# Kernel optimization log

Hardware: AMD Instinct MI355X
Metric: run time of the kernel (lower is better)

The kernel has to match this reference:

```python
import jax, jax.numpy as jnp
import numpy as np

N_NODES = 50000
NEG_SLOPE = 0.2  # PyG GATConv default leaky_relu slope


def setup_inputs() -> dict:
    key = jax.random.key(0)
    ks = jax.random.split(key, 12)
    N, E, D_IN, H = N_NODES, 1200000, 128, 64
    sd_in = 1.0 / np.sqrt(D_IN)
    sd_h = 1.0 / np.sqrt(H)
    return {
        "x": jax.random.normal(ks[0], (N, D_IN), jnp.float32),
        "src": jax.random.randint(ks[1], (E,), 0, N, jnp.int32),
        "dst": jax.random.randint(ks[2], (E,), 0, N, jnp.int32),
        "W1_src": jax.random.normal(ks[3], (D_IN, H), jnp.float32) * sd_in,
        "W1_dst": jax.random.normal(ks[4], (D_IN, H), jnp.float32) * sd_in,
        "a1_src": jax.random.normal(ks[5], (H,), jnp.float32) * sd_h,
        "a1_dst": jax.random.normal(ks[6], (H,), jnp.float32) * sd_h,
        "b1": jnp.zeros((H,), jnp.float32),
        "W2_src": jax.random.normal(ks[7], (H, H), jnp.float32) * sd_h,
        "W2_dst": jax.random.normal(ks[8], (H, H), jnp.float32) * sd_h,
        "a2_src": jax.random.normal(ks[9], (H,), jnp.float32) * sd_h,
        "a2_dst": jax.random.normal(ks[10], (H,), jnp.float32) * sd_h,
        "b2": jnp.zeros((H,), jnp.float32),
    }


def _gat_layer(x, src, dst, W_src, W_dst, att_src, att_dst, bias):
    N = x.shape[0]
    h_src = x @ W_src            # [N, H] transformed source features
    h_dst = x @ W_dst            # [N, H] transformed destination features
    alpha_src = h_src @ att_src  # [N]
    alpha_dst = h_dst @ att_dst  # [N]
    # edge-wise attention logits (gather), edge j -> i: e = lrelu(a_src[j] + a_dst[i])
    e = jax.nn.leaky_relu(alpha_src[src] + alpha_dst[dst], NEG_SLOPE)  # [E]
    # segment softmax over incoming edges of each destination node
    m = jax.ops.segment_max(e, dst, num_segments=N)          # [N]
    ex = jnp.exp(e - m[dst])                                  # [E]
    denom = jax.ops.segment_sum(ex, dst, num_segments=N)     # [N]
    alpha = ex / denom[dst]                                   # [E]
    # weighted scatter-add aggregation
    msgs = h_src[src] * alpha[:, None]                        # [E, H]
    out = jax.ops.segment_sum(msgs, dst, num_segments=N)     # [N, H]
    return out + bias


def reference(x, src, dst, W1_src, W1_dst, a1_src, a1_dst, b1,
              W2_src, W2_dst, a2_src, a2_dst, b2):
    h = jnp.tanh(_gat_layer(x, src, dst, W1_src, W1_dst, a1_src, a1_dst, b1))
    h = jnp.tanh(_gat_layer(h, src, dst, W2_src, W2_dst, a2_src, a2_dst, b2))
    return h
```

## Files before the change

### kernel.cpp

```cpp
#include <hip/hip_runtime.h>
#include <hip/hip_bf16.h>

#define NEG_SLOPE 0.2f
#define EPB 4096
#define NHB 64

typedef __attribute__((ext_vector_type(8))) short short8v;
typedef __attribute__((ext_vector_type(4))) float f32x4;

__device__ inline float blo(unsigned u) { return __uint_as_float(u << 16); }
__device__ inline float bhi(unsigned u) { return __uint_as_float(u & 0xffff0000u); }
__device__ inline unsigned short bf16bits(float f) {
    __hip_bfloat16 b = __float2bfloat16(f);
    return *(unsigned short*)&b;
}
__device__ inline unsigned pack2bf(float e, float o) {
    return ((unsigned)bf16bits(o) << 16) | (unsigned)bf16bits(e);
}

template <int K>
__device__ inline void stage_sBt(unsigned short* sBt,
                                 const float* __restrict__ W_src,
                                 const float* __restrict__ a_src,
                                 const float* __restrict__ W_dst,
                                 const float* __restrict__ a_dst, int tid) {
    constexpr int PAD = K + 8;
    for (int i = tid; i < 64 * K; i += 256) {
        int k = i >> 6, j = i & 63;
        sBt[j * PAD + k] = bf16bits(W_src[i]);
    }
    for (int i = tid; i < 2 * K; i += 256) {
        int which = (i >= K) ? 1 : 0;
        int k = i - which * K;
        const float* Wr = (which ? W_dst : W_src) + k * 64;
        const float* av = which ? a_dst : a_src;
        float s = 0.f;
        #pragma unroll
        for (int j = 0; j < 64; ++j) s += Wr[j] * av[j];
        sBt[(64 + which) * PAD + k] = bf16bits(s);
    }
    for (int i = tid; i < 14 * K; i += 256) {
        int j = 66 + i / K, k = i % K;
        sBt[j * PAD + k] = 0;
    }
}

template <int K>
__device__ inline void nt_mfma_body(const unsigned short* sBt,
                                    const unsigned short* sX,
                                    int rowblockbase,
                                    unsigned* __restrict__ hb_out,
                                    float* __restrict__ alpha_src,
                                    float* __restrict__ alpha_dst,
                                    int N, int tid) {
    constexpr int PAD = K + 8;
    int wid = tid >> 6, l = tid & 63;
    int jcol = l & 15;

    f32x4 acc[5];
    #pragma unroll
    for (int t = 0; t < 5; ++t) acc[t] = (f32x4){0.f, 0.f, 0.f, 0.f};

    const unsigned short* xrow = &sX[(wid * 16 + (l & 15)) * PAD + (l >> 4) * 8];
    #pragma unroll
    for (int kt = 0; kt < K / 32; ++kt) {
        short8v a = *(const short8v*)(xrow + kt * 32);
        int kbase = kt * 32 + (l >> 4) * 8;
        #pragma unroll
        for (int t = 0; t < 5; ++t) {
            short8v b = *(const short8v*)&sBt[(t * 16 + jcol) * PAD + kbase];
            acc[t] = __builtin_amdgcn_mfma_f32_16x16x32_bf16(a, b, acc[t], 0, 0, 0);
        }
    }

    int rbase = rowblockbase + wid * 16 + (l >> 4) * 4;
    #pragma unroll
    for (int t = 0; t < 4; ++t) {
        #pragma unroll
        for (int r = 0; r < 4; ++r) {
            float v = acc[t][r];
            float w = __shfl_xor(v, 1);
            int row = rbase + r;
            if (!(l & 1) && row < N)
                hb_out[(size_t)row * 32 + t * 8 + (jcol >> 1)] = pack2bf(v, w);
        }
    }
    #pragma unroll
    for (int r = 0; r < 4; ++r) {
        int row = rbase + r;
        if (row < N) {
            if (jcol == 0) alpha_src[row] = acc[4][r];
            if (jcol == 1) alpha_dst[row] = acc[4][r];
        }
    }
}

__global__ __launch_bounds__(256) void fused_nt1_hist(
    const float* __restrict__ x,
    const float* __restrict__ W_src, const float* __restrict__ a_src,
    const float* __restrict__ W_dst, const float* __restrict__ a_dst,
    unsigned* __restrict__ hb_out, float* __restrict__ alpha_src,
    float* __restrict__ alpha_dst, int N,
    const int* __restrict__ dst, int* __restrict__ partials, int E, int ntb) {
    constexpr int K = 128, PAD = K + 8;
    __shared__ unsigned short sBt[80 * PAD];
    __shared__ unsigned short sX[64 * PAD];
    __shared__ int lh[256];
    int tid = threadIdx.x;

    if ((int)blockIdx.x >= ntb) {
        int bh = blockIdx.x - ntb;
        lh[tid] = 0;
        __syncthreads();
        for (int e = bh * 256 + tid; e < E; e += NHB * 256)
            atomicAdd(&lh[dst[e] >> 8], 1);
        __syncthreads();
        partials[bh * 256 + tid] = lh[tid];
        return;
    }

    stage_sBt<K>(sBt, W_src, a_src, W_dst, a_dst, tid);
    for (int idx = tid; idx < 64 * K / 4; idx += 256) {
        int row = (idx * 4) / K, col = (idx * 4) % K;
        int g = blockIdx.x * 64 + row;
        const float4 f = *(const float4*)(x + (size_t)((g < N) ? g : N - 1) * K + col);
        unsigned short* d = &sX[row * PAD + col];
        d[0] = bf16bits(f.x); d[1] = bf16bits(f.y);
        d[2] = bf16bits(f.z); d[3] = bf16bits(f.w);
    }
    __syncthreads();
    nt_mfma_body<K>(sBt, sX, blockIdx.x * 64, hb_out, alpha_src, alpha_dst, N, tid);
}

__global__ __launch_bounds__(256) void bucket_scan(const int* __restrict__ partials,
                                                   int* __restrict__ bucket_base,
                                                   int* __restrict__ bucket_cursor) {
    __shared__ int tmp[256];
    int tid = threadIdx.x;
    int v = 0;
    #pragma unroll 8
    for (int b = 0; b < NHB; ++b) v += partials[b * 256 + tid];
    tmp[tid] = v;
    __syncthreads();
    for (int off = 1; off < 256; off <<= 1) {
        int t = (tid >= off) ? tmp[tid - off] : 0;
        __syncthreads();
        tmp[tid] += t;
        __syncthreads();
    }
    int excl = tmp[tid] - v;
    bucket_base[tid] = excl;
    bucket_cursor[tid] = excl;
    if (tid == 255) bucket_base[256] = tmp[255];
}

__global__ __launch_bounds__(256) void bucket_scatter(const int* __restrict__ src,
                                                      const int* __restrict__ dst,
                                                      int* __restrict__ bucket_cursor,
                                                      unsigned* __restrict__ ebuf, int E) {
    __shared__ int lhist[256];
    __shared__ int lbase[256];
    int tid = threadIdx.x;
    lhist[tid] = 0;
    __syncthreads();
    int base = blockIdx.x * EPB;
    int bkt[16], rank[16];
    unsigned pack[16];
    #pragma unroll
    for (int i = 0; i < 16; ++i) {
        int e = base + i * 256 + tid;
        bkt[i] = -1;
        if (e < E) {
            int d = dst[e], s = src[e];
            bkt[i]  = d >> 8;
            pack[i] = ((unsigned)(d & 255) << 16) | (unsigned)s;
            rank[i] = atomicAdd(&lhist[bkt[i]], 1);
        }
    }
    __syncthreads();
    int cnt = lhist[tid];
    if (cnt) lbase[tid] = atomicAdd(&bucket_cursor[tid], cnt);
    __syncthreads();
    #pragma unroll
    for (int i = 0; i < 16; ++i)
        if (bkt[i] >= 0) ebuf[lbase[bkt[i]] + rank[i]] = pack[i];
}

__global__ __launch_bounds__(256) void bucket_build(const unsigned* __restrict__ ebuf,
                                                    const int* __restrict__ bucket_base,
                                                    int* __restrict__ row_ptr,
                                                    int* __restrict__ csr_src,
                                                    int N, int E) {
    __shared__ int deg[256];
    __shared__ int cur[256];
    __shared__ int tmp[256];
    int b = blockIdx.x, tid = threadIdx.x;
    int ebase = bucket_base[b], eend = bucket_base[b + 1];
    deg[tid] = 0;
    __syncthreads();
    for (int e = ebase + tid; e < eend; e += 256)
        atomicAdd(&deg[ebuf[e] >> 16], 1);
    __syncthreads();
    int v = deg[tid];
    tmp[tid] = v;
    __syncthreads();
    for (int off = 1; off < 256; off <<= 1) {
        int t = (tid >= off) ? tmp[tid - off] : 0;
        __syncthreads();
        tmp[tid] += t;
        __syncthreads();
    }
    int excl = tmp[tid] - v;
    int node = b * 256 + tid;
    if (node < N) row_ptr[node] = ebase + excl;
    if (b == 0 && tid == 0) row_ptr[N] = E;
    cur[tid] = excl;
    __syncthreads();
    for (int e = ebase + tid; e < eend; e += 256) {
        unsigned pk = ebuf[e];
        int r = atomicAdd(&cur[pk >> 16], 1);
        csr_src[ebase + r] = (int)(pk & 0xFFFFu);
    }
}

__device__ inline float agg_node(int node, const int* __restrict__ row_ptr,
                                 const int* __restrict__ csr_src,
                                 const float* __restrict__ alpha_src,
                                 const float* __restrict__ alpha_dst,
                                 const unsigned* __restrict__ hb,
                                 float blane, int lane) {
    int beg = row_ptr[node], end = row_ptr[node + 1];
    float adst = alpha_dst[node];
    int half = lane >> 5, sub = lane & 31;

    float dL = 0.f;
    float aA[4] = {0.f, 0.f, 0.f, 0.f};
    float aB[4] = {0.f, 0.f, 0.f, 0.f};

    for (int c = beg; c < end; c += 64) {
        int cnt = end - c;
        cnt = (cnt < 64) ? cnt : 64;

        int s = 0;
        float p = 0.f;
        if (lane < cnt) {
            s = csr_src[c + lane];
            float t = alpha_src[s] + adst;
            t = (t > 0.f) ? t : NEG_SLOPE * t;
            p = __expf(fminf(t, 60.f));
            dL += p;
        }

        for (int j = 0; j < cnt; j += 16) {
            int   sv[8];
            float pv[8];
            unsigned uv[8];
            #pragma unroll
            for (int i = 0; i < 8; ++i) {
                int e = j + 2 * i + half;
                sv[i] = __shfl(s, e);
                pv[i] = __shfl(p, e);
            }
            #pragma unroll
            for (int i = 0; i < 8; ++i)
                uv[i] = hb[(size_t)sv[i] * 32 + sub];
            #pragma unroll
            for (int i = 0; i < 8; ++i) {
                aA[i & 3] = fmaf(pv[i], blo(uv[i]), aA[i & 3]);
                aB[i & 3] = fmaf(pv[i], bhi(uv[i]), aB[i & 3]);
            }
        }
    }
    float denom = dL;
    #pragma unroll
    for (int off = 32; off; off >>= 1) denom += __shfl_xor(denom, off);

    float accA = (aA[0] + aA[1]) + (aA[2] + aA[3]);
    float accB = (aB[0] + aB[1]) + (aB[2] + aB[3]);
    accA += __shfl_xor(accA, 32);
    accB += __shfl_xor(accB, 32);
    int srcl = lane >> 1;
    float vA = __shfl(accA, srcl);
    float vB = __shfl(accB, srcl);
    float val = (lane & 1) ? vB : vA;
    float r = (denom > 0.f) ? (val / denom) : 0.f;
    return tanhf(r + blane);
}

__global__ __launch_bounds__(256) void fused_agg_nt(
    const int* __restrict__ row_ptr, const int* __restrict__ csr_src,
    const float* __restrict__ alpha_src1, const float* __restrict__ alpha_dst1,
    const unsigned* __restrict__ hb1,
    const float* __restrict__ bias1,
    const float* __restrict__ W_src, const float* __restrict__ a_src,
    const float* __restrict__ W_dst, const float* __restrict__ a_dst,
    unsigned* __restrict__ hb2, float* __restrict__ alpha_src2,
    float* __restrict__ alpha_dst2, int N) {
    constexpr int K = 64, PAD = K + 8;
    __shared__ unsigned short sBt[80 * PAD];
    __shared__ unsigned short sX[64 * PAD];
    int tid = threadIdx.x;

    stage_sBt<K>(sBt, W_src, a_src, W_dst, a_dst, tid);

    int wid = tid >> 6, lane = tid & 63;
    int blockbase = blockIdx.x * 64;
    float blane = bias1[lane];

    for (int i = 0; i < 16; ++i) {
        int node = blockbase + wid * 16 + i;
        float fv = 0.f;
        if (node < N)
            fv = agg_node(node, row_ptr, csr_src, alpha_src1, alpha_dst1, hb1,
                          blane, lane);
        sX[(wid * 16 + i) * PAD + lane] = bf16bits(fv);
    }
    __syncthreads();
    nt_mfma_body<K>(sBt, sX, blockbase, hb2, alpha_src2, alpha_dst2, N, tid);
}

__global__ __launch_bounds__(256) void aggregate_out(
    const int* __restrict__ row_ptr, const int* __restrict__ csr_src,
    const float* __restrict__ alpha_src, const float* __restrict__ alpha_dst,
    const unsigned* __restrict__ hb, const float* __restrict__ bias,
    float* __restrict__ out, int N) {
    int wid = threadIdx.x >> 6, lane = threadIdx.x & 63;
    int node = blockIdx.x * 4 + wid;
    if (node >= N) return;
    float fv = agg_node(node, row_ptr, csr_src, alpha_src, alpha_dst, hb,
                        bias[lane], lane);
    out[(size_t)node * 64 + lane] = fv;
}

extern "C" void kernel_launch(void* const* d_in, const int* in_sizes, int n_in,
                              void* d_out, int out_size, void* d_ws, size_t ws_size,
                              hipStream_t stream) {
    const float* x      = (const float*)d_in[0];
    const int*   src    = (const int*)  d_in[1];
    const int*   dst    = (const int*)  d_in[2];
    const float* W1_src = (const float*)d_in[3];
    const float* W1_dst = (const float*)d_in[4];
    const float* a1_src = (const float*)d_in[5];
    const float* a1_dst = (const float*)d_in[6];
    const float* b1     = (const float*)d_in[7];
    const float* W2_src = (const float*)d_in[8];
    const float* W2_dst = (const float*)d_in[9];
    const float* a2_src = (const float*)d_in[10];
    const float* a2_dst = (const float*)d_in[11];
    const float* b2     = (const float*)d_in[12];
    float* out = (float*)d_out;

    const int N = in_sizes[0] / 128;
    const int E = in_sizes[1];
    const int NB = (N + 255) / 256;

    char* ws = (char*)d_ws;
    size_t off = 0;
    auto alloc = [&](size_t bytes) {
        void* p = ws + off;
        off += (bytes + 255) & ~(size_t)255;
        return p;
    };
    unsigned* hbuf1   = (unsigned*)alloc((size_t)N * 32 * 4);
    unsigned* hbuf2   = (unsigned*)alloc((size_t)N * 32 * 4);
    float* alpha_s1   = (float*)alloc((size_t)N * 4);
    float* alpha_d1   = (float*)alloc((size_t)N * 4);
    float* alpha_s2   = (float*)alloc((size_t)N * 4);
    float* alpha_d2   = (float*)alloc((size_t)N * 4);
    int*   row_ptr    = (int*)  alloc((size_t)(N + 1) * 4);
    int*   csr_src    = (int*)  alloc((size_t)E * 4);
    int*   partials   = (int*)  alloc(NHB * 256 * 4);
    int*   bucket_base   = (int*)alloc(257 * 4);
    int*   bucket_cursor = (int*)alloc(256 * 4);
    unsigned* ebuf    = (unsigned*)alloc((size_t)E * 4);
    (void)ws_size; (void)NB;

    const int eb3  = (E + EPB - 1) / EPB;
    const int aggb = (N + 3) / 4;
    const int ntb  = (N + 63) / 64;

    fused_nt1_hist<<<ntb + NHB, 256, 0, stream>>>(
        x, W1_src, a1_src, W1_dst, a1_dst, hbuf1, alpha_s1, alpha_d1, N,
        dst, partials, E, ntb);
    bucket_scan<<<1, 256, 0, stream>>>(partials, bucket_base, bucket_cursor);
    bucket_scatter<<<eb3, 256, 0, stream>>>(src, dst, bucket_cursor, ebuf, E);
    bucket_build<<<NB, 256, 0, stream>>>(ebuf, bucket_base, row_ptr, csr_src, N, E);
    fused_agg_nt<<<ntb, 256, 0, stream>>>(
        row_ptr, csr_src, alpha_s1, alpha_d1, hbuf1, b1,
        W2_src, a2_src, W2_dst, a2_dst, hbuf2, alpha_s2, alpha_d2, N);
    aggregate_out<<<aggb, 256, 0, stream>>>(
        row_ptr, csr_src, alpha_s2, alpha_d2, hbuf2, b2, out, N);
}
```

Measured before the change: 154.8 us.

## Split aggregation into logits pass and two feature-half gather passes

Replaces the fused aggregate+transform kernel with separate kernels. A logits kernel precomputes normalized attention per edge into a buffer. Two gather kernels each handle one half of the feature columns, so each pass touches a smaller part of the bf16 feature table and may fit it better in cache. A standalone bf16 MFMA transform kernel then builds the layer-2 inputs. The cost is more launches, an extra E-sized write and read of alpha, and csr_src being read three times per layer.

```diff
diff --git a/kernel.cpp b/kernel.cpp
--- a/kernel.cpp
+++ b/kernel.cpp
@@ -132,6 +132,28 @@
     nt_mfma_body<K>(sBt, sX, blockIdx.x * 64, hb_out, alpha_src, alpha_dst, N, tid);
 }
 
+template <int K>
+__global__ __launch_bounds__(256) void nt_bf16(
+    const unsigned short* __restrict__ x,
+    const float* __restrict__ W_src, const float* __restrict__ a_src,
+    const float* __restrict__ W_dst, const float* __restrict__ a_dst,
+    unsigned* __restrict__ hb_out, float* __restrict__ alpha_src,
+    float* __restrict__ alpha_dst, int N) {
+    constexpr int PAD = K + 8;
+    __shared__ unsigned short sBt[80 * PAD];
+    __shared__ unsigned short sX[64 * PAD];
+    int tid = threadIdx.x;
+    stage_sBt<K>(sBt, W_src, a_src, W_dst, a_dst, tid);
+    for (int idx = tid; idx < 64 * K / 8; idx += 256) {
+        int row = (idx * 8) / K, col = (idx * 8) % K;
+        int g = blockIdx.x * 64 + row;
+        short8v v = *(const short8v*)(x + (size_t)((g < N) ? g : N - 1) * K + col);
+        *(short8v*)&sX[row * PAD + col] = v;
+    }
+    __syncthreads();
+    nt_mfma_body<K>(sBt, sX, blockIdx.x * 64, hb_out, alpha_src, alpha_dst, N, tid);
+}
+
 __global__ __launch_bounds__(256) void bucket_scan(const int* __restrict__ partials,
                                                    int* __restrict__ bucket_base,
                                                    int* __restrict__ bucket_cursor) {
@@ -223,113 +245,120 @@
     }
 }
 
-__device__ inline float agg_node(int node, const int* __restrict__ row_ptr,
-                                 const int* __restrict__ csr_src,
-                                 const float* __restrict__ alpha_src,
-                                 const float* __restrict__ alpha_dst,
-                                 const unsigned* __restrict__ hb,
-                                 float blane, int lane) {
+__global__ __launch_bounds__(256) void agg_logits(
+    const int* __restrict__ row_ptr, const int* __restrict__ csr_src,
+    const float* __restrict__ alpha_src, const float* __restrict__ alpha_dst,
+    float* __restrict__ palpha, int N) {
+    int wid = threadIdx.x >> 6, lane = threadIdx.x & 63;
+    int node = blockIdx.x * 4 + wid;
+    if (node >= N) return;
     int beg = row_ptr[node], end = row_ptr[node + 1];
     float adst = alpha_dst[node];
-    int half = lane >> 5, sub = lane & 31;
-
-    float dL = 0.f;
+    int deg = end - beg;
+
+    if (deg <= 64) {
+        float p = 0.f;
+        if (lane < deg) {
+            int s = __builtin_nontemporal_load(&csr_src[beg + lane]);
+            float t = alpha_src[s] + adst;
+            t = (t > 0.f) ? t : NEG_SLOPE * t;
+            p = __expf(fminf(t, 60.f));
+        }
+        float denom = p;
+        #pragma unroll
+        for (int off = 32; off; off >>= 1) denom += __shfl_xor(denom, off);
+        float inv = (denom > 0.f) ? 1.f / denom : 0.f;
+        if (lane < deg)
+            __builtin_nontemporal_store(p * inv, &palpha[beg + lane]);
+    } else {
+        float dL = 0.f;
+        for (int c = beg; c < end; c += 64) {
+            int e = c + lane;
+            if (e < end) {
+                int s = __builtin_nontemporal_load(&csr_src[e]);
+                float t = alpha_src[s] + adst;
+                t = (t > 0.f) ? t : NEG_SLOPE * t;
+                float p = __expf(fminf(t, 60.f));
+                palpha[e] = p;
+                dL += p;
+            }
+        }
+        float denom = dL;
+        #pragma unroll
+        for (int off = 32; off; off >>= 1) denom += __shfl_xor(denom, off);
+        float inv = (denom > 0.f) ? 1.f / denom : 0.f;
+        for (int c = beg; c < end; c += 64) {
+            int e = c + lane;
+            if (e < end) palpha[e] *= inv;
+        }
+    }
+}
+
+template <int HALF, bool OUTBF16>
+__global__ __launch_bounds__(256) void agg_gather(
+    const int* __restrict__ row_ptr, const int* __restrict__ csr_src,
+    const float* __restrict__ palpha,
+    const unsigned* __restrict__ hb,
+    const float* __restrict__ bias,
+    void* __restrict__ out_, int N) {
+    int wid = threadIdx.x >> 6, lane = threadIdx.x & 63;
+    int node = blockIdx.x * 4 + wid;
+    if (node >= N) return;
+    int beg = row_ptr[node], end = row_ptr[node + 1];
+    int grp = lane >> 4, sub = lane & 15;
+    const unsigned* hbh = hb + HALF * 16;
+
     float aA[4] = {0.f, 0.f, 0.f, 0.f};
     float aB[4] = {0.f, 0.f, 0.f, 0.f};
 
     for (int c = beg; c < end; c += 64) {
         int cnt = end - c;
         cnt = (cnt < 64) ? cnt : 64;
-
         int s = 0;
-        float p = 0.f;
+        float a = 0.f;
         if (lane < cnt) {
-            s = csr_src[c + lane];
-            float t = alpha_src[s] + adst;
-            t = (t > 0.f) ? t : NEG_SLOPE * t;
-            p = __expf(fminf(t, 60.f));
-            dL += p;
-        }
-
-        for (int j = 0; j < cnt; j += 16) {
-            int   sv[8];
-            float pv[8];
+            s = __builtin_nontemporal_load(&csr_src[c + lane]);
+            a = __builtin_nontemporal_load(&palpha[c + lane]);
+        }
+        for (int j = 0; j < cnt; j += 32) {
+            int sv[8];
+            float av[8];
             unsigned uv[8];
             #pragma unroll
             for (int i = 0; i < 8; ++i) {
-                int e = j + 2 * i + half;
+                int e = j + 4 * i + grp;
                 sv[i] = __shfl(s, e);
-                pv[i] = __shfl(p, e);
+                av[i] = __shfl(a, e);
             }
             #pragma unroll
             for (int i = 0; i < 8; ++i)
-                uv[i] = hb[(size_t)sv[i] * 32 + sub];
+                uv[i] = hbh[(size_t)sv[i] * 32 + sub];
             #pragma unroll
             for (int i = 0; i < 8; ++i) {
-                aA[i & 3] = fmaf(pv[i], blo(uv[i]), aA[i & 3]);
-                aB[i & 3] = fmaf(pv[i], bhi(uv[i]), aB[i & 3]);
+                aA[i & 3] = fmaf(av[i], blo(uv[i]), aA[i & 3]);
+                aB[i & 3] = fmaf(av[i], bhi(uv[i]), aB[i & 3]);
             }
         }
     }
-    float denom = dL;
-    #pragma unroll
-    for (int off = 32; off; off >>= 1) denom += __shfl_xor(denom, off);
-
-    float accA = (aA[0] + aA[1]) + (aA[2] + aA[3]);
-    float accB = (aB[0] + aB[1]) + (aB[2] + aB[3]);
-    accA += __shfl_xor(accA, 32);
-    accB += __shfl_xor(accB, 32);
-    int srcl = lane >> 1;
-    float vA = __shfl(accA, srcl);
-    float vB = __shfl(accB, srcl);
-    float val = (lane & 1) ? vB : vA;
-    float r = (denom > 0.f) ? (val / denom) : 0.f;
-    return tanhf(r + blane);
-}
-
-__global__ __launch_bounds__(256) void fused_agg_nt(
-    const int* __restrict__ row_ptr, const int* __restrict__ csr_src,
-    const float* __restrict__ alpha_src1, const float* __restrict__ alpha_dst1,
-    const unsigned* __restrict__ hb1,
-    const float* __restrict__ bias1,
-    const float* __restrict__ W_src, const float* __restrict__ a_src,
-    const float* __restrict__ W_dst, const float* __restrict__ a_dst,
-    unsigned* __restrict__ hb2, float* __restrict__ alpha_src2,
-    float* __restrict__ alpha_dst2, int N) {
-    constexpr int K = 64, PAD = K + 8;
-    __shared__ unsigned short sBt[80 * PAD];
-    __shared__ unsigned short sX[64 * PAD];
-    int tid = threadIdx.x;
-
-    stage_sBt<K>(sBt, W_src, a_src, W_dst, a_dst, tid);
-
-    int wid = tid >> 6, lane = tid & 63;
-    int blockbase = blockIdx.x * 64;
-    float blane = bias1[lane];
-
-    for (int i = 0; i < 16; ++i) {
-        int node = blockbase + wid * 16 + i;
-        float fv = 0.f;
-        if (node < N)
-            fv = agg_node(node, row_ptr, csr_src, alpha_src1, alpha_dst1, hb1,
-                          blane, lane);
-        sX[(wid * 16 + i) * PAD + lane] = bf16bits(fv);
-    }
-    __syncthreads();
-    nt_mfma_body<K>(sBt, sX, blockbase, hb2, alpha_src2, alpha_dst2, N, tid);
-}
-
-__global__ __launch_bounds__(256) void aggregate_out(
-    const int* __restrict__ row_ptr, const int* __restrict__ csr_src,
-    const float* __restrict__ alpha_src, const float* __restrict__ alpha_dst,
-    const unsigned* __restrict__ hb, const float* __restrict__ bias,
-    float* __restrict__ out, int N) {
-    int wid = threadIdx.x >> 6, lane = threadIdx.x & 63;
-    int node = blockIdx.x * 4 + wid;
-    if (node >= N) return;
-    float fv = agg_node(node, row_ptr, csr_src, alpha_src, alpha_dst, hb,
-                        bias[lane], lane);
-    out[(size_t)node * 64 + lane] = fv;
+    float A = (aA[0] + aA[1]) + (aA[2] + aA[3]);
+    float B = (aB[0] + aB[1]) + (aB[2] + aB[3]);
+    A += __shfl_xor(A, 16); A += __shfl_xor(A, 32);
+    B += __shfl_xor(B, 16); B += __shfl_xor(B, 32);
+
+    int f0 = HALF * 32 + 2 * sub;
+    float v0 = tanhf(A + bias[f0]);
+    float v1 = tanhf(B + bias[f0 + 1]);
+
+    if (grp == 0) {
+        if constexpr (OUTBF16) {
+            __builtin_nontemporal_store(pack2bf(v0, v1),
+                (unsigned*)out_ + (size_t)node * 32 + HALF * 16 + sub);
+        } else {
+            float* op = (float*)out_ + (size_t)node * 64 + f0;
+            __builtin_nontemporal_store(v0, op);
+            __builtin_nontemporal_store(v1, op + 1);
+        }
+    }
 }
 
 extern "C" void kernel_launch(void* const* d_in, const int* in_sizes, int n_in,
@@ -361,22 +390,24 @@
         off += (bytes + 255) & ~(size_t)255;
         return p;
     };
-    unsigned* hbuf1   = (unsigned*)alloc((size_t)N * 32 * 4);
-    unsigned* hbuf2   = (unsigned*)alloc((size_t)N * 32 * 4);
-    float* alpha_s1   = (float*)alloc((size_t)N * 4);
-    float* alpha_d1   = (float*)alloc((size_t)N * 4);
-    float* alpha_s2   = (float*)alloc((size_t)N * 4);
-    float* alpha_d2   = (float*)alloc((size_t)N * 4);
-    int*   row_ptr    = (int*)  alloc((size_t)(N + 1) * 4);
-    int*   csr_src    = (int*)  alloc((size_t)E * 4);
-    int*   partials   = (int*)  alloc(NHB * 256 * 4);
+    unsigned* hbuf1  = (unsigned*)alloc((size_t)N * 32 * 4);
+    unsigned* h1buf  = (unsigned*)alloc((size_t)N * 32 * 4);
+    unsigned* hbuf2  = (unsigned*)alloc((size_t)N * 32 * 4);
+    float* alpha_s1  = (float*)alloc((size_t)N * 4);
+    float* alpha_d1  = (float*)alloc((size_t)N * 4);
+    float* alpha_s2  = (float*)alloc((size_t)N * 4);
+    float* alpha_d2  = (float*)alloc((size_t)N * 4);
+    float* palpha    = (float*)alloc((size_t)E * 4);
+    int*   row_ptr   = (int*)  alloc((size_t)(N + 1) * 4);
+    int*   csr_src   = (int*)  alloc((size_t)E * 4);
+    int*   partials  = (int*)  alloc(NHB * 256 * 4);
     int*   bucket_base   = (int*)alloc(257 * 4);
     int*   bucket_cursor = (int*)alloc(256 * 4);
-    unsigned* ebuf    = (unsigned*)alloc((size_t)E * 4);
-    (void)ws_size; (void)NB;
+    unsigned* ebuf   = (unsigned*)alloc((size_t)E * 4);
+    (void)ws_size;
 
     const int eb3  = (E + EPB - 1) / EPB;
-    const int aggb = (N + 3) / 4;
+    const int nwb  = (N + 3) / 4;
     const int ntb  = (N + 63) / 64;
 
     fused_nt1_hist<<<ntb + NHB, 256, 0, stream>>>(
@@ -385,9 +416,21 @@
     bucket_scan<<<1, 256, 0, stream>>>(partials, bucket_base, bucket_cursor);
     bucket_scatter<<<eb3, 256, 0, stream>>>(src, dst, bucket_cursor, ebuf, E);
     bucket_build<<<NB, 256, 0, stream>>>(ebuf, bucket_base, row_ptr, csr_src, N, E);
-    fused_agg_nt<<<ntb, 256, 0, stream>>>(
-        row_ptr, csr_src, alpha_s1, alpha_d1, hbuf1, b1,
-        W2_src, a2_src, W2_dst, a2_dst, hbuf2, alpha_s2, alpha_d2, N);
-    aggregate_out<<<aggb, 256, 0, stream>>>(
-        row_ptr, csr_src, alpha_s2, alpha_d2, hbuf2, b2, out, N);
-}
+
+    agg_logits<<<nwb, 256, 0, stream>>>(row_ptr, csr_src, alpha_s1, alpha_d1,
+                                        palpha, N);
+    agg_gather<0, true><<<nwb, 256, 0, stream>>>(row_ptr, csr_src, palpha,
+                                                 hbuf1, b1, h1buf, N);
+    agg_gather<1, true><<<nwb, 256, 0, stream>>>(row_ptr, csr_src, palpha,
+                                                 hbuf1, b1, h1buf, N);
+
+    nt_bf16<64><<<ntb, 256, 0, stream>>>((const unsigned short*)h1buf,
+                                         W2_src, a2_src, W2_dst, a2_dst,
+                                         hbuf2, alpha_s2, alpha_d2, N);
+    agg_logits<<<nwb, 256, 0, stream>>>(row_ptr, csr_src, alpha_s2, alpha_d2,
+                                        palpha, N);
+    agg_gather<0, false><<<nwb, 256, 0, stream>>>(row_ptr, csr_src, palpha,
+                                                  hbuf2, b2, out, N);
+    agg_gather<1, false><<<nwb, 256, 0, stream>>>(row_ptr, csr_src, palpha,
+                                                  hbuf2, b2, out, N);
+}
```

New measurement: 205.3 us. 1.33x slower.
